# Optimization experiments

Hardware: AMD Instinct MI355X
Metric: run time of the kernel (lower is better)

## Reference

```python
import jax, jax.numpy as jnp
import numpy as np

B, T, I, H = 512, 512, 64, 256


def _gru_layer(x, w_ih, w_hh, b_ih, b_hh):
    # x: [B, T, in]; w_ih: [3H, in]; w_hh: [3H, H]; gate order r, z, n (PyTorch)
    xg = jnp.einsum('bti,gi->btg', x, w_ih) + b_ih  # [B, T, 3H], input projections for all steps
    xg = jnp.swapaxes(xg, 0, 1)  # [T, B, 3H] for scan over time
    h0 = jnp.zeros((x.shape[0], w_hh.shape[1]), dtype=x.dtype)

    def step(h, xg_t):
        hg = h @ w_hh.T + b_hh  # [B, 3H]
        xr, xz, xn = jnp.split(xg_t, 3, axis=-1)
        hr, hz, hn = jnp.split(hg, 3, axis=-1)
        r = jax.nn.sigmoid(xr + hr)
        z = jax.nn.sigmoid(xz + hz)
        n = jnp.tanh(xn + r * hn)
        h_new = (1.0 - z) * n + z * h
        return h_new, h_new

    h_last, ys = jax.lax.scan(step, h0, xg)
    return jnp.swapaxes(ys, 0, 1), h_last  # [B, T, H], [B, H]


def setup_inputs() -> dict:
    key = jax.random.key(0)
    ks = jax.random.split(key, 11)
    s_in = 1.0 / np.sqrt(H)
    x = jax.random.normal(ks[0], (B, T, I), dtype=jnp.float32)
    w_ih0 = jax.random.uniform(ks[1], (3 * H, I), jnp.float32, -s_in, s_in)
    w_hh0 = jax.random.uniform(ks[2], (3 * H, H), jnp.float32, -s_in, s_in)
    b_ih0 = jax.random.uniform(ks[3], (3 * H,), jnp.float32, -s_in, s_in)
    b_hh0 = jax.random.uniform(ks[4], (3 * H,), jnp.float32, -s_in, s_in)
    w_ih1 = jax.random.uniform(ks[5], (3 * H, H), jnp.float32, -s_in, s_in)
    w_hh1 = jax.random.uniform(ks[6], (3 * H, H), jnp.float32, -s_in, s_in)
    b_ih1 = jax.random.uniform(ks[7], (3 * H,), jnp.float32, -s_in, s_in)
    b_hh1 = jax.random.uniform(ks[8], (3 * H,), jnp.float32, -s_in, s_in)
    w_lin = jax.random.uniform(ks[9], (1, H), jnp.float32, -s_in, s_in)
    b_lin = jax.random.uniform(ks[10], (1,), jnp.float32, -s_in, s_in)
    return dict(x=x, w_ih0=w_ih0, w_hh0=w_hh0, b_ih0=b_ih0, b_hh0=b_hh0,
                w_ih1=w_ih1, w_hh1=w_hh1, b_ih1=b_ih1, b_hh1=b_hh1,
                w_lin=w_lin, b_lin=b_lin)


def reference(x, w_ih0, w_hh0, b_ih0, b_hh0, w_ih1, w_hh1, b_ih1, b_hh1, w_lin, b_lin):
    y0, h_last0 = _gru_layer(x, w_ih0, w_hh0, b_ih0, b_hh0)
    # dropout(0.2) between layers is inactive at inference -> identity
    y1, h_last1 = _gru_layer(y0, w_ih1, w_hh1, b_ih1, b_hh1)
    # original uses hn[0] = final hidden of LAYER 0
    logits = (h_last0 @ w_lin.T + b_lin).reshape(-1)  # [B]
    p = jax.nn.sigmoid(logits)
    out = jnp.stack((p, 1.0 - p), axis=1).reshape(-1)  # [2B]
    return out
```

## Files before the change

### kernel.cpp

```cpp
#include <hip/hip_runtime.h>


typedef __attribute__((ext_vector_type(8))) short short8;
typedef __attribute__((ext_vector_type(4))) float floatx4;

#define T_LEN 512
#define I_DIM 64
#define H_DIM 256
#define NB 16
#define NWG 32
#define L2E 1.4426950408889634f

#define HSTATE_OFF 131072
#define XG_OFF     1048576
#define XG_PER_T   786432ull
#define XG_TSTRIDE 393216

__device__ __forceinline__ unsigned short f2bf(float f) {
    union { float f; unsigned u; } v; v.f = f;
    return (unsigned short)((v.u + 0x7FFFu + ((v.u >> 16) & 1u)) >> 16);
}

__device__ __forceinline__ float bf2f(unsigned short u) {
    union { unsigned u; float f; } v; v.u = ((unsigned)u) << 16;
    return v.f;
}

__device__ __forceinline__ short8 pack8v(floatx4 a, floatx4 b) {
    short8 r;
    r[0] = (short)f2bf(a[0]); r[1] = (short)f2bf(a[1]);
    r[2] = (short)f2bf(a[2]); r[3] = (short)f2bf(a[3]);
    r[4] = (short)f2bf(b[0]); r[5] = (short)f2bf(b[1]);
    r[6] = (short)f2bf(b[2]); r[7] = (short)f2bf(b[3]);
    return r;
}

__device__ __forceinline__ short8 pack8s(const float* p, float s) {
    floatx4 a = *(const floatx4*)p;
    floatx4 b = *(const floatx4*)(p + 4);
    short8 r;
    r[0] = (short)f2bf(a[0] * s); r[1] = (short)f2bf(a[1] * s);
    r[2] = (short)f2bf(a[2] * s); r[3] = (short)f2bf(a[3] * s);
    r[4] = (short)f2bf(b[0] * s); r[5] = (short)f2bf(b[1] * s);
    r[6] = (short)f2bf(b[2] * s); r[7] = (short)f2bf(b[3] * s);
    return r;
}

__device__ __forceinline__ float sigm(float a) {
    return 1.0f / (1.0f + __expf(-a));
}

__global__ void cvt_wih_kernel(const float* __restrict__ w,
                               unsigned short* __restrict__ o) {
    int i = blockIdx.x * 256 + threadIdx.x;
    if (i < 6144) {
        const int l  = i & 63;
        const int kx = (i >> 6) & 1;
        const int g  = (i >> 7) % 6;
        const int wv = (i >> 7) / 6;
        const int row = (g >> 1) * 256 + wv * 32 + (g & 1) * 16 + (l & 15);
        const int col = kx * 32 + (l >> 4) * 8;
        const float* p = w + row * I_DIM + col;
        *(short8*)&o[i * 8] = pack8v(*(const floatx4*)p,
                                     *(const floatx4*)(p + 4));
    }
}

__global__ __launch_bounds__(256) void xg_kernel(
    const float* __restrict__ x,
    const unsigned short* __restrict__ wih_bf,
    unsigned short* __restrict__ xg,
    const float* __restrict__ b_ih,
    const float* __restrict__ b_hh,
    int t0)
{
    const int tid  = threadIdx.x;
    const int wv   = tid >> 6;
    const int lane = tid & 63;
    const int m16  = lane & 15;
    const int quad = lane >> 4;
    const int wgb  = blockIdx.x & 31;
    const int tl0  = (blockIdx.x >> 5) * 16 + wv * 4;

    short8 af0[4], af1[4];
    #pragma unroll
    for (int j = 0; j < 4; ++j) {
        const float* xp = x + ((long)(wgb * 16 + m16) * T_LEN + (t0 + tl0 + j))
                              * I_DIM + quad * 8;
        af0[j] = pack8v(*(const floatx4*)xp,        *(const floatx4*)(xp + 4));
        af1[j] = pack8v(*(const floatx4*)(xp + 32), *(const floatx4*)(xp + 36));
    }

    #pragma unroll 1
    for (int wp = 0; wp < 8; ++wp) {
        #pragma unroll 1
        for (int gate = 0; gate < 3; ++gate) {
            const int u0 = wp * 32 + m16;
            float bs0, bs1, sc;
            if (gate < 2) {
                bs0 = b_ih[gate * 256 + u0]      + b_hh[gate * 256 + u0];
                bs1 = b_ih[gate * 256 + u0 + 16] + b_hh[gate * 256 + u0 + 16];
                sc  = L2E;
            } else {
                bs0 = b_ih[512 + u0];
                bs1 = b_ih[512 + u0 + 16];
                sc  = 2.0f * L2E;
            }
            const int gb = (wp * 6 + gate * 2) * 2;
            short8 b00 = *(const short8*)&wih_bf[((gb + 0) * 64 + lane) * 8];
            short8 b01 = *(const short8*)&wih_bf[((gb + 1) * 64 + lane) * 8];
            short8 b10 = *(const short8*)&wih_bf[((gb + 2) * 64 + lane) * 8];
            short8 b11 = *(const short8*)&wih_bf[((gb + 3) * 64 + lane) * 8];
            #pragma unroll
            for (int j = 0; j < 4; ++j) {
                floatx4 a0 = {0, 0, 0, 0}, a1 = {0, 0, 0, 0};
                a0 = __builtin_amdgcn_mfma_f32_16x16x32_bf16(af0[j], b00, a0, 0, 0, 0);
                a0 = __builtin_amdgcn_mfma_f32_16x16x32_bf16(af1[j], b01, a0, 0, 0, 0);
                a1 = __builtin_amdgcn_mfma_f32_16x16x32_bf16(af0[j], b10, a1, 0, 0, 0);
                a1 = __builtin_amdgcn_mfma_f32_16x16x32_bf16(af1[j], b11, a1, 0, 0, 0);
                short8 pk;
                pk[0] = (short)f2bf((a0[0] + bs0) * sc);
                pk[1] = (short)f2bf((a0[1] + bs0) * sc);
                pk[2] = (short)f2bf((a0[2] + bs0) * sc);
                pk[3] = (short)f2bf((a0[3] + bs0) * sc);
                pk[4] = (short)f2bf((a1[0] + bs1) * sc);
                pk[5] = (short)f2bf((a1[1] + bs1) * sc);
                pk[6] = (short)f2bf((a1[2] + bs1) * sc);
                pk[7] = (short)f2bf((a1[3] + bs1) * sc);
                long off = ((((long)(tl0 + j) * 32 + wgb) * 3 + gate) * 512
                            + wp * 64 + lane) * 8;
                *(short8*)&xg[off] = pk;
            }
        }
    }
}

__global__ __launch_bounds__(512, 2) void gru_scan8(
    const unsigned short* __restrict__ xg,
    const float* __restrict__ w_hh,
    const float* __restrict__ b_hh,
    const float* __restrict__ w_lin,
    const float* __restrict__ b_lin,
    float* __restrict__ h_state,
    float* __restrict__ out,
    int t0, int tlen, int last)
{
    __shared__ __align__(16) unsigned short hbf[1024 * 8];

    const int tid  = threadIdx.x;
    const int wave = tid >> 6;
    const int lane = tid & 63;
    const int m16  = lane & 15;
    const int quad = lane >> 4;
    const int wg   = blockIdx.x;

    for (int b = tid; b < 1024; b += 512)
        *(short8*)&hbf[b * 8] = (short8)0;

    float h_old[8] = {0, 0, 0, 0, 0, 0, 0, 0};
    if (t0 > 0) {
        unsigned short* hbn = &hbf[(t0 & 1) * 512 * 8];
        #pragma unroll
        for (int i = 0; i < 2; ++i) {
            #pragma unroll
            for (int r = 0; r < 4; ++r) {
                float v = h_state[(long)(wg * NB + quad * 4 + r) * H_DIM
                                  + wave * 32 + i * 16 + m16];
                h_old[i * 4 + r] = v;
                hbn[(wave * 64 + (i * 2 + (m16 >> 3)) * 16 + quad * 4 + r) * 8
                    + (m16 & 7)] = f2bf(v);
            }
        }
    }

    short8 whh[3][2][8];
    #pragma unroll
    for (int g = 0; g < 3; ++g) {
        const float sc = (g < 2) ? L2E : 2.0f * L2E;
        #pragma unroll
        for (int i = 0; i < 2; ++i) {
            const float* rp = w_hh
                + (long)(g * 256 + wave * 32 + i * 16 + m16) * H_DIM;
            #pragma unroll
            for (int k = 0; k < 8; ++k)
                whh[g][i][k] = pack8s(rp + k * 32 + quad * 8, sc);
        }
    }
    float anb[2];
    anb[0] = 2.0f * L2E * b_hh[512 + wave * 32 + m16];
    anb[1] = 2.0f * L2E * b_hh[512 + wave * 32 + 16 + m16];

    const unsigned short* xgb = xg + (long)wg * 12288 + tid * 8;
    short8 pf0 = *(const short8*)&xgb[0];
    short8 pf1 = *(const short8*)&xgb[4096];
    short8 xnc = *(const short8*)&xgb[8192];
    const unsigned short* xgn = xgb + XG_TSTRIDE;

    if (wave >= 4) __builtin_amdgcn_s_setprio(1);

    __syncthreads();

    #pragma unroll 1
    for (int tt = 0; tt < tlen; ++tt) {
        const int t = t0 + tt;
        floatx4 aR[2], aZ[2], aN[2];
        #pragma unroll
        for (int i = 0; i < 2; ++i) {
            #pragma unroll
            for (int r = 0; r < 4; ++r) {
                aR[i][r] = bf2f((unsigned short)pf0[i * 4 + r]);
                aZ[i][r] = bf2f((unsigned short)pf1[i * 4 + r]);
            }
            aN[i] = (floatx4){anb[i], anb[i], anb[i], anb[i]};
        }
        pf0 = *(const short8*)&xgn[0];
        pf1 = *(const short8*)&xgn[4096];

        const unsigned short* hb = &hbf[(t & 1) * 512 * 8];

        #pragma unroll
        for (int k = 0; k < 8; ++k) {
            short8 af = *(const short8*)&hb[(k * 64 + lane) * 8];
            aR[0] = __builtin_amdgcn_mfma_f32_16x16x32_bf16(af, whh[0][0][k], aR[0], 0, 0, 0);
            aR[1] = __builtin_amdgcn_mfma_f32_16x16x32_bf16(af, whh[0][1][k], aR[1], 0, 0, 0);
            aZ[0] = __builtin_amdgcn_mfma_f32_16x16x32_bf16(af, whh[1][0][k], aZ[0], 0, 0, 0);
            aZ[1] = __builtin_amdgcn_mfma_f32_16x16x32_bf16(af, whh[1][1][k], aZ[1], 0, 0, 0);
        }

        #pragma unroll
        for (int k = 0; k < 8; ++k) {
            short8 af = *(const short8*)&hb[(k * 64 + lane) * 8];
            aN[0] = __builtin_amdgcn_mfma_f32_16x16x32_bf16(af, whh[2][0][k], aN[0], 0, 0, 0);
            aN[1] = __builtin_amdgcn_mfma_f32_16x16x32_bf16(af, whh[2][1][k], aN[1], 0, 0, 0);
        }

        float rr[8], zh[8], omz[8], xf[8];
        #pragma unroll
        for (int i = 0; i < 2; ++i) {
            #pragma unroll
            for (int r = 0; r < 4; ++r) {
                const int e = i * 4 + r;
                rr[e]  = __builtin_amdgcn_rcpf(1.0f + __builtin_amdgcn_exp2f(-aR[i][r]));
                float zz = __builtin_amdgcn_rcpf(1.0f + __builtin_amdgcn_exp2f(-aZ[i][r]));
                zh[e]  = zz * h_old[e];
                omz[e] = 1.0f - zz;
                xf[e]  = bf2f((unsigned short)xnc[i * 4 + r]);
            }
        }

        unsigned short* hbn = &hbf[((t + 1) & 1) * 512 * 8];
        #pragma unroll
        for (int i = 0; i < 2; ++i) {
            float hv0, hv1, hv2, hv3;
            #pragma unroll
            for (int r = 0; r < 4; ++r) {
                const int e = i * 4 + r;
                float av = xf[e] + rr[e] * aN[i][r];
                float tn = 1.0f - 2.0f * __builtin_amdgcn_rcpf(1.0f + __builtin_amdgcn_exp2f(av));
                float hv = omz[e] * tn + zh[e];
                h_old[e] = hv;
                if (r == 0) hv0 = hv; else if (r == 1) hv1 = hv;
                else if (r == 2) hv2 = hv; else hv3 = hv;
            }
            unsigned pk0, pk1;
            asm("v_cvt_pk_bf16_f32 %0, %1, %2" : "=v"(pk0) : "v"(hv0), "v"(hv1));
            asm("v_cvt_pk_bf16_f32 %0, %1, %2" : "=v"(pk1) : "v"(hv2), "v"(hv3));
            unsigned short* wb = &hbn[(wave * 64 + (i * 2 + (m16 >> 3)) * 16
                                       + quad * 4) * 8 + (m16 & 7)];
            wb[0]  = (unsigned short)(pk0 & 0xffffu);
            wb[8]  = (unsigned short)(pk0 >> 16);
            wb[16] = (unsigned short)(pk1 & 0xffffu);
            wb[24] = (unsigned short)(pk1 >> 16);
        }

        xnc = *(const short8*)&xgn[8192];
        if (tt < tlen - 2) xgn += XG_TSTRIDE;

        asm volatile("s_waitcnt lgkmcnt(0)" ::: "memory");
        __builtin_amdgcn_s_barrier();
    }

    if (wave >= 4) __builtin_amdgcn_s_setprio(0);

    #pragma unroll
    for (int i = 0; i < 2; ++i)
        #pragma unroll
        for (int r = 0; r < 4; ++r)
            h_state[(long)(wg * NB + quad * 4 + r) * H_DIM
                    + wave * 32 + i * 16 + m16] = h_old[i * 4 + r];

    if (!last) return;

    __syncthreads();
    float* hfin = (float*)hbf;
    #pragma unroll
    for (int i = 0; i < 2; ++i)
        #pragma unroll
        for (int r = 0; r < 4; ++r)
            hfin[(quad * 4 + r) * 256 + wave * 32 + i * 16 + m16] =
                h_old[i * 4 + r];
    __syncthreads();

    const int m = tid >> 5, j = tid & 31;
    float s = 0.0f;
    #pragma unroll
    for (int c = 0; c < 8; ++c)
        s += hfin[m * 256 + j + c * 32] * w_lin[j + c * 32];
    #pragma unroll
    for (int d = 16; d > 0; d >>= 1) s += __shfl_down(s, d, 32);
    if (j == 0) {
        float p = sigm(s + b_lin[0]);
        const int b = wg * NB + m;
        out[2 * b]     = p;
        out[2 * b + 1] = 1.0f - p;
    }
}

__global__ __launch_bounds__(512, 1) void gru_kernel(
    const float* __restrict__ x,
    const float* __restrict__ w_hh,
    const float* __restrict__ b_ih,
    const float* __restrict__ b_hh,
    const unsigned short* __restrict__ wih_ws,
    const float* __restrict__ w_lin,
    const float* __restrict__ b_lin,
    float* __restrict__ out)
{
    __shared__ __align__(16) unsigned short whn_lds[8192 * 8];
    __shared__ __align__(16) unsigned short hbf[1024 * 8];
    __shared__ __align__(16) unsigned short bias_lds[512 * 8];

    const int tid  = threadIdx.x;
    const int wave = tid >> 6;
    const int lane = tid & 63;
    const int m16  = lane & 15;
    const int quad = lane >> 4;
    const int wg   = blockIdx.x;

    for (int b = tid; b < 8192; b += 512) {
        const int l = b & 63;
        const int k = (b >> 6) & 7;
        const int g = (b >> 9) & 1;
        const int w = b >> 10;
        const int row = 512 + w * 32 + g * 16 + (l & 15);
        const int col = k * 32 + (l >> 4) * 8;
        const float* p = w_hh + row * H_DIM + col;
        *(short8*)&whn_lds[b * 8] = pack8v(*(const floatx4*)p,
                                           *(const floatx4*)(p + 4));
    }
    for (int b = tid; b < 1024; b += 512)
        *(short8*)&hbf[b * 8] = (short8)0;

    {
        const int u0 = wave * 32 + m16, u1 = u0 + 16;
        unsigned short* bl = &bias_lds[tid * 8];
        bl[0] = f2bf(b_ih[u0] + b_hh[u0]);
        bl[1] = f2bf(b_ih[u1] + b_hh[u1]);
        bl[2] = f2bf(b_ih[256 + u0] + b_hh[256 + u0]);
        bl[3] = f2bf(b_ih[256 + u1] + b_hh[256 + u1]);
        bl[4] = f2bf(b_hh[512 + u0]);
        bl[5] = f2bf(b_hh[512 + u1]);
        bl[6] = f2bf(b_ih[512 + u0]);
        bl[7] = f2bf(b_ih[512 + u1]);
    }

    short8 whh[4][8];
    #pragma unroll
    for (int g = 0; g < 4; ++g) {
        const int row = (g >> 1) * 256 + wave * 32 + (g & 1) * 16 + m16;
        const float* rp = w_hh + row * H_DIM;
        #pragma unroll
        for (int k = 0; k < 8; ++k) {
            const float* p = rp + k * 32 + quad * 8;
            whh[g][k] = pack8v(*(const floatx4*)p, *(const floatx4*)(p + 4));
        }
    }

    short8 wi[12];
    {
        const unsigned short* wib = &wih_ws[(wave * 6 * 2 * 64 + lane) * 8];
        #pragma unroll
        for (int j = 0; j < 12; ++j)
            wi[j] = *(const short8*)&wib[j * 64 * 8];
    }

    float h_old[8] = {0, 0, 0, 0, 0, 0, 0, 0};
    const float* xbase = x + (long)(wg * NB + m16) * T_LEN * I_DIM + quad * 8;

    __syncthreads();

    #pragma unroll 1
    for (int t = 0; t < T_LEN; ++t) {
        const float* xt = xbase + t * I_DIM;
        floatx4 x0 = *(const floatx4*)(xt);
        floatx4 x1 = *(const floatx4*)(xt + 4);
        floatx4 x2 = *(const floatx4*)(xt + 32);
        floatx4 x3 = *(const floatx4*)(xt + 36);

        floatx4 acc[4], an[2], xnl[2];
        #pragma unroll
        for (int g = 0; g < 4; ++g) acc[g] = (floatx4){0, 0, 0, 0};
        an[0] = an[1] = xnl[0] = xnl[1] = (floatx4){0, 0, 0, 0};

        const unsigned short* hb  = &hbf[(t & 1) * 512 * 8];
        const unsigned short* wnb = &whn_lds[(wave * 2 * 8 * 64 + lane) * 8];
        #pragma unroll
        for (int k = 0; k < 8; ++k) {
            short8 af  = *(const short8*)&hb[(k * 64 + lane) * 8];
            short8 wn0 = *(const short8*)&wnb[(k * 64) * 8];
            short8 wn1 = *(const short8*)&wnb[((8 + k) * 64) * 8];
            acc[0] = __builtin_amdgcn_mfma_f32_16x16x32_bf16(af, whh[0][k], acc[0], 0, 0, 0);
            acc[1] = __builtin_amdgcn_mfma_f32_16x16x32_bf16(af, whh[1][k], acc[1], 0, 0, 0);
            acc[2] = __builtin_amdgcn_mfma_f32_16x16x32_bf16(af, whh[2][k], acc[2], 0, 0, 0);
            acc[3] = __builtin_amdgcn_mfma_f32_16x16x32_bf16(af, whh[3][k], acc[3], 0, 0, 0);
            an[0]  = __builtin_amdgcn_mfma_f32_16x16x32_bf16(af, wn0, an[0], 0, 0, 0);
            an[1]  = __builtin_amdgcn_mfma_f32_16x16x32_bf16(af, wn1, an[1], 0, 0, 0);
        }

        short8 xa = pack8v(x0, x1);
        acc[0] = __builtin_amdgcn_mfma_f32_16x16x32_bf16(xa, wi[0],  acc[0], 0, 0, 0);
        acc[1] = __builtin_amdgcn_mfma_f32_16x16x32_bf16(xa, wi[2],  acc[1], 0, 0, 0);
        acc[2] = __builtin_amdgcn_mfma_f32_16x16x32_bf16(xa, wi[4],  acc[2], 0, 0, 0);
        acc[3] = __builtin_amdgcn_mfma_f32_16x16x32_bf16(xa, wi[6],  acc[3], 0, 0, 0);
        xnl[0] = __builtin_amdgcn_mfma_f32_16x16x32_bf16(xa, wi[8],  xnl[0], 0, 0, 0);
        xnl[1] = __builtin_amdgcn_mfma_f32_16x16x32_bf16(xa, wi[10], xnl[1], 0, 0, 0);
        xa = pack8v(x2, x3);
        acc[0] = __builtin_amdgcn_mfma_f32_16x16x32_bf16(xa, wi[1],  acc[0], 0, 0, 0);
        acc[1] = __builtin_amdgcn_mfma_f32_16x16x32_bf16(xa, wi[3],  acc[1], 0, 0, 0);
        acc[2] = __builtin_amdgcn_mfma_f32_16x16x32_bf16(xa, wi[5],  acc[2], 0, 0, 0);
        acc[3] = __builtin_amdgcn_mfma_f32_16x16x32_bf16(xa, wi[7],  acc[3], 0, 0, 0);
        xnl[0] = __builtin_amdgcn_mfma_f32_16x16x32_bf16(xa, wi[9],  xnl[0], 0, 0, 0);
        xnl[1] = __builtin_amdgcn_mfma_f32_16x16x32_bf16(xa, wi[11], xnl[1], 0, 0, 0);

        short8 bv = *(const short8*)&bias_lds[tid * 8];
        unsigned short* hbn = &hbf[((t + 1) & 1) * 512 * 8];
        #pragma unroll
        for (int i = 0; i < 2; ++i) {
            #pragma unroll
            for (int r = 0; r < 4; ++r) {
                const int idx = i * 4 + r;
                float rr = sigm(acc[i][r]     + bf2f((unsigned short)bv[i]));
                float zz = sigm(acc[2 + i][r] + bf2f((unsigned short)bv[2 + i]));
                float av = xnl[i][r] + bf2f((unsigned short)bv[6 + i])
                         + rr * (an[i][r] + bf2f((unsigned short)bv[4 + i]));
                float nn = 1.0f - 2.0f / (1.0f + __expf(2.0f * av));
                float hn = (1.0f - zz) * nn + zz * h_old[idx];
                h_old[idx] = hn;
                hbn[(wave * 64 + (i * 2 + (m16 >> 3)) * 16 + quad * 4 + r) * 8
                    + (m16 & 7)] = f2bf(hn);
            }
        }
        __syncthreads();
    }

    __syncthreads();
    float* hfin = (float*)hbf;
    #pragma unroll
    for (int i = 0; i < 2; ++i)
        #pragma unroll
        for (int r = 0; r < 4; ++r)
            hfin[(quad * 4 + r) * 256 + wave * 32 + i * 16 + m16] =
                h_old[i * 4 + r];
    __syncthreads();

    const int m = tid >> 5, j = tid & 31;
    float s = 0.0f;
    #pragma unroll
    for (int c = 0; c < 8; ++c)
        s += hfin[m * 256 + j + c * 32] * w_lin[j + c * 32];
    #pragma unroll
    for (int d = 16; d > 0; d >>= 1) s += __shfl_down(s, d, 32);
    if (j == 0) {
        float p = sigm(s + b_lin[0]);
        const int b = wg * NB + m;
        out[2 * b]     = p;
        out[2 * b + 1] = 1.0f - p;
    }
}

extern "C" void kernel_launch(void* const* d_in, const int* in_sizes, int n_in,
                              void* d_out, int out_size, void* d_ws, size_t ws_size,
                              hipStream_t stream) {
    const float* x     = (const float*)d_in[0];
    const float* w_ih0 = (const float*)d_in[1];
    const float* w_hh0 = (const float*)d_in[2];
    const float* b_ih0 = (const float*)d_in[3];
    const float* b_hh0 = (const float*)d_in[4];
    const float* w_lin = (const float*)d_in[9];
    const float* b_lin = (const float*)d_in[10];
    float* out = (float*)d_out;

    unsigned short* wih_bf = (unsigned short*)d_ws;
    cvt_wih_kernel<<<24, 256, 0, stream>>>(w_ih0, wih_bf);

    int Tc = 0;
    for (int c = 512; c >= 32; c >>= 1)
        if (ws_size >= XG_OFF + (size_t)c * XG_PER_T) { Tc = c; break; }

    if (Tc) {
        float* h_state = (float*)((char*)d_ws + HSTATE_OFF);
        unsigned short* xg = (unsigned short*)((char*)d_ws + XG_OFF);
        for (int t0 = 0; t0 < T_LEN; t0 += Tc) {
            xg_kernel<<<32 * (Tc / 16), 256, 0, stream>>>(x, wih_bf, xg,
                                                          b_ih0, b_hh0, t0);
            gru_scan8<<<NWG, 512, 0, stream>>>(xg, w_hh0, b_hh0,
                                               w_lin, b_lin, h_state, out,
                                               t0, Tc, (t0 + Tc == T_LEN) ? 1 : 0);
        }
    } else {
        gru_kernel<<<NWG, 512, 0, stream>>>(x, w_hh0, b_ih0, b_hh0, wih_bf,
                                            w_lin, b_lin, out);
    }
}
```

Baseline: 1.037 ms.

## Pre-convert W_hh to bf16, overlap gate sigmoids with N-gate MFMAs, cap chunk size

A new kernel converts W_hh to pre-scaled bf16 in MFMA fragment order once, so each scan workgroup loads ready fragments instead of converting fp32 weights. Inside the step loop, the r/z sigmoids are computed before the n-gate MFMA chain so transcendental work can overlap the matrix ops, and the h update is refactored to fewer ops. Wave priority boosting is removed and the time chunk is capped at 256, giving two chunked launches where one may have run before, which adds launch and state save/restore overhead.

```diff
diff --git a/kernel.cpp b/kernel.cpp
--- a/kernel.cpp
+++ b/kernel.cpp
@@ -12,6 +12,7 @@
 #define L2E 1.4426950408889634f
 
 #define HSTATE_OFF 131072
+#define WHH_OFF    655360
 #define XG_OFF     1048576
 #define XG_PER_T   786432ull
 #define XG_TSTRIDE 393216
@@ -63,6 +64,22 @@
         const float* p = w + row * I_DIM + col;
         *(short8*)&o[i * 8] = pack8v(*(const floatx4*)p,
                                      *(const floatx4*)(p + 4));
+    }
+}
+
+__global__ void cvt_whh_kernel(const float* __restrict__ w,
+                               unsigned short* __restrict__ o) {
+    int i = blockIdx.x * 256 + threadIdx.x;
+    if (i < 24576) {
+        const int lane = i & 63;
+        const int k  = (i >> 6) & 7;
+        const int ii = (i >> 9) & 1;
+        const int g  = (i >> 10) % 3;
+        const int wv = (i >> 10) / 3;
+        const int row = g * 256 + wv * 32 + ii * 16 + (lane & 15);
+        const int col = k * 32 + (lane >> 4) * 8;
+        const float sc = (g < 2) ? L2E : 2.0f * L2E;
+        *(short8*)&o[i * 8] = pack8s(w + (long)row * H_DIM + col, sc);
     }
 }
 
@@ -137,7 +154,7 @@
 
 __global__ __launch_bounds__(512, 2) void gru_scan8(
     const unsigned short* __restrict__ xg,
-    const float* __restrict__ w_hh,
+    const unsigned short* __restrict__ whh_bf,
     const float* __restrict__ b_hh,
     const float* __restrict__ w_lin,
     const float* __restrict__ b_lin,
@@ -174,17 +191,16 @@
     }
 
     short8 whh[3][2][8];
-    #pragma unroll
-    for (int g = 0; g < 3; ++g) {
-        const float sc = (g < 2) ? L2E : 2.0f * L2E;
-        #pragma unroll
-        for (int i = 0; i < 2; ++i) {
-            const float* rp = w_hh
-                + (long)(g * 256 + wave * 32 + i * 16 + m16) * H_DIM;
-            #pragma unroll
-            for (int k = 0; k < 8; ++k)
-                whh[g][i][k] = pack8s(rp + k * 32 + quad * 8, sc);
-        }
+    {
+        const unsigned short* wb = &whh_bf[((long)wave * 48 * 64 + lane) * 8];
+        #pragma unroll
+        for (int g = 0; g < 3; ++g)
+            #pragma unroll
+            for (int i = 0; i < 2; ++i)
+                #pragma unroll
+                for (int k = 0; k < 8; ++k)
+                    whh[g][i][k] = *(const short8*)
+                        &wb[(((g * 2 + i) * 8 + k) * 64) * 8];
     }
     float anb[2];
     anb[0] = 2.0f * L2E * b_hh[512 + wave * 32 + m16];
@@ -195,8 +211,6 @@
     short8 pf1 = *(const short8*)&xgb[4096];
     short8 xnc = *(const short8*)&xgb[8192];
     const unsigned short* xgn = xgb + XG_TSTRIDE;
-
-    if (wave >= 4) __builtin_amdgcn_s_setprio(1);
 
     __syncthreads();
 
@@ -228,36 +242,32 @@
         }
 
         #pragma unroll
+        for (int i = 0; i < 2; ++i) {
+            #pragma unroll
+            for (int r = 0; r < 4; ++r) {
+                aR[i][r] = __builtin_amdgcn_rcpf(1.0f + __builtin_amdgcn_exp2f(-aR[i][r]));
+                aZ[i][r] = __builtin_amdgcn_rcpf(1.0f + __builtin_amdgcn_exp2f(-aZ[i][r]));
+            }
+        }
+
+        #pragma unroll
         for (int k = 0; k < 8; ++k) {
             short8 af = *(const short8*)&hb[(k * 64 + lane) * 8];
             aN[0] = __builtin_amdgcn_mfma_f32_16x16x32_bf16(af, whh[2][0][k], aN[0], 0, 0, 0);
             aN[1] = __builtin_amdgcn_mfma_f32_16x16x32_bf16(af, whh[2][1][k], aN[1], 0, 0, 0);
         }
 
-        float rr[8], zh[8], omz[8], xf[8];
+        unsigned short* hbn = &hbf[((t + 1) & 1) * 512 * 8];
         #pragma unroll
         for (int i = 0; i < 2; ++i) {
+            float hv0, hv1, hv2, hv3;
             #pragma unroll
             for (int r = 0; r < 4; ++r) {
                 const int e = i * 4 + r;
-                rr[e]  = __builtin_amdgcn_rcpf(1.0f + __builtin_amdgcn_exp2f(-aR[i][r]));
-                float zz = __builtin_amdgcn_rcpf(1.0f + __builtin_amdgcn_exp2f(-aZ[i][r]));
-                zh[e]  = zz * h_old[e];
-                omz[e] = 1.0f - zz;
-                xf[e]  = bf2f((unsigned short)xnc[i * 4 + r]);
-            }
-        }
-
-        unsigned short* hbn = &hbf[((t + 1) & 1) * 512 * 8];
-        #pragma unroll
-        for (int i = 0; i < 2; ++i) {
-            float hv0, hv1, hv2, hv3;
-            #pragma unroll
-            for (int r = 0; r < 4; ++r) {
-                const int e = i * 4 + r;
-                float av = xf[e] + rr[e] * aN[i][r];
+                float xnv = bf2f((unsigned short)xnc[i * 4 + r]);
+                float av = xnv + aR[i][r] * aN[i][r];
                 float tn = 1.0f - 2.0f * __builtin_amdgcn_rcpf(1.0f + __builtin_amdgcn_exp2f(av));
-                float hv = omz[e] * tn + zh[e];
+                float hv = tn + aZ[i][r] * (h_old[e] - tn);
                 h_old[e] = hv;
                 if (r == 0) hv0 = hv; else if (r == 1) hv1 = hv;
                 else if (r == 2) hv2 = hv; else hv3 = hv;
@@ -279,8 +289,6 @@
         asm volatile("s_waitcnt lgkmcnt(0)" ::: "memory");
         __builtin_amdgcn_s_barrier();
     }
-
-    if (wave >= 4) __builtin_amdgcn_s_setprio(0);
 
     #pragma unroll
     for (int i = 0; i < 2; ++i)
@@ -494,18 +502,21 @@
     cvt_wih_kernel<<<24, 256, 0, stream>>>(w_ih0, wih_bf);
 
     int Tc = 0;
-    for (int c = 512; c >= 32; c >>= 1)
+    for (int c = 256; c >= 32; c >>= 1)
         if (ws_size >= XG_OFF + (size_t)c * XG_PER_T) { Tc = c; break; }
 
     if (Tc) {
         float* h_state = (float*)((char*)d_ws + HSTATE_OFF);
+        unsigned short* whh_bf = (unsigned short*)((char*)d_ws + WHH_OFF);
         unsigned short* xg = (unsigned short*)((char*)d_ws + XG_OFF);
+        cvt_whh_kernel<<<96, 256, 0, stream>>>(w_hh0, whh_bf);
         for (int t0 = 0; t0 < T_LEN; t0 += Tc) {
             xg_kernel<<<32 * (Tc / 16), 256, 0, stream>>>(x, wih_bf, xg,
                                                           b_ih0, b_hh0, t0);
-            gru_scan8<<<NWG, 512, 0, stream>>>(xg, w_hh0, b_hh0,
+            gru_scan8<<<NWG, 512, 0, stream>>>(xg, whh_bf, b_hh0,
                                                w_lin, b_lin, h_state, out,
-                                               t0, Tc, (t0 + Tc == T_LEN) ? 1 : 0);
+                                               t0, Tc,
+                                               (t0 + Tc >= T_LEN) ? 1 : 0);
         }
     } else {
         gru_kernel<<<NWG, 512, 0, stream>>>(x, w_hh0, b_ih0, b_hh0, wih_bf,
```

New measurement: 859.2 us. 17.2% less time.
